# Kernel tuning notes

Measured on AMD Instinct MI355X. Metric: run time of the kernel, lower is better.

## Reference

```python
import jax, jax.numpy as jnp
import numpy as np

N = 131072   # query points
K = 32       # top-k gaussians per point
G = 100000   # num_gaussians
DELTA = 0.05
EPS = 1e-8


def setup_inputs() -> dict:
    key = jax.random.key(0)
    ks = jax.random.split(key, 7)
    coords = jax.random.normal(ks[0], (N, 3), jnp.float32) * 2.0
    # PSF covariance: symmetric PSD per point (A A^T + 0.1 I)
    A = jax.random.normal(ks[1], (N, 3, 3), jnp.float32) * 0.3
    Sigma_psf = jnp.einsum('nij,nkj->nik', A, A) + 0.1 * jnp.eye(3, dtype=jnp.float32)
    mu = jax.random.normal(ks[2], (G, 3), jnp.float32) * 2.0
    scaling = jax.random.uniform(ks[3], (G, 3), jnp.float32, minval=0.5, maxval=1.5)
    rotation_g = jax.random.normal(ks[4], (G, 4), jnp.float32)
    color = jax.random.uniform(ks[5], (G,), jnp.float32)
    top_k_idcs = jax.random.randint(ks[6], (N, K), 0, G)
    return {"coords": coords, "Sigma_psf": Sigma_psf, "mu": mu, "scaling": scaling,
            "rotation_g": rotation_g, "color": color, "top_k_idcs": top_k_idcs}


def _quat_to_rot(q):
    # q: (G,4) wxyz -> R: (G,3,3), matches fused kernel math (rsqrt normalize)
    inv_norm = jax.lax.rsqrt(jnp.sum(q * q, axis=-1, keepdims=True) + EPS)
    qn = q * inv_norm
    w, x, y, z = qn[..., 0], qn[..., 1], qn[..., 2], qn[..., 3]
    x2, y2, z2 = x * x, y * y, z * z
    xy, xz, yz = x * y, x * z, y * z
    wx, wy, wz = w * x, w * y, w * z
    r0 = jnp.stack([1.0 - 2.0 * (y2 + z2), 2.0 * (xy - wz), 2.0 * (xz + wy)], axis=-1)
    r1 = jnp.stack([2.0 * (xy + wz), 1.0 - 2.0 * (x2 + z2), 2.0 * (yz - wx)], axis=-1)
    r2 = jnp.stack([2.0 * (xz - wy), 2.0 * (yz + wx), 1.0 - 2.0 * (x2 + y2)], axis=-1)
    return jnp.stack([r0, r1, r2], axis=-2)


def _compute_sigma(scaling, rotation_g, scale_scale):
    # Sigma = R diag(s^2) R^T, s = scaling * scale_scale
    R = _quat_to_rot(rotation_g)            # (G,3,3)
    M = R * (scaling * scale_scale)[:, None, :]  # scale columns
    return jnp.einsum('gik,gjk->gij', M, M)      # (G,3,3)


def _mahalanobis(sig, v):
    # sig: (N,K,3,3) symmetric; v: (N,K,3). Explicit 3x3 inverse, same as torch kernel.
    a = sig[..., 0, 0]; b = sig[..., 0, 1]; c = sig[..., 0, 2]
    e = sig[..., 1, 1]; f = sig[..., 1, 2]
    h = sig[..., 2, 1]; i = sig[..., 2, 2]
    det = a * (e * i - f * h) - b * (b * i - f * c) + c * (b * h - e * c)
    inv_det = 1.0 / (det + EPS)
    inv00 = (e * i - f * h) * inv_det
    inv01 = (c * h - b * i) * inv_det
    inv02 = (b * f - c * e) * inv_det
    inv11 = (a * i - c * c) * inv_det
    inv12 = (c * b - a * f) * inv_det
    inv22 = (a * e - b * b) * inv_det
    vx, vy, vz = v[..., 0], v[..., 1], v[..., 2]
    t0 = inv00 * vx + inv01 * vy + inv02 * vz
    t1 = inv01 * vx + inv11 * vy + inv12 * vz
    t2 = inv02 * vx + inv12 * vy + inv22 * vz
    return vx * t0 + vy * t1 + vz * t2


def reference(coords, Sigma_psf, mu, scaling, rotation_g, color, top_k_idcs):
    scale_scale = 1.0  # default; thresholding branch inactive
    mus = mu[top_k_idcs]                         # (N,K,3)
    x_minus_mu = coords[:, None, :] - mus        # (N,K,3)
    sigmas = _compute_sigma(scaling, rotation_g, scale_scale)[top_k_idcs]  # (N,K,3,3)
    sigmas = (sigmas + Sigma_psf[:, None, :, :]).astype(jnp.float32)
    inner = _mahalanobis(sigmas, x_minus_mu)     # (N,K)
    w = jnp.exp(-0.5 * inner)
    sum_w = jnp.sum(w, axis=1, keepdims=True)
    w_nrmd = w / (sum_w + DELTA)
    intensity = jnp.sum(w_nrmd * color[top_k_idcs], axis=1)  # (N,)
    return intensity
```

## Files before the change

### kernel.cpp

```cpp
#include <hip/hip_runtime.h>
#include <hip/hip_fp16.h>

#define DELTA 0.05f
#define EPS 1e-8f

union H2F { __half2 h; float f; };

__global__ __launch_bounds__(256) void precompute_gauss(
    const float* __restrict__ mu,
    const float* __restrict__ scaling,
    const float* __restrict__ rot,
    const float* __restrict__ color,
    float4* __restrict__ table, int G)
{
    int g = blockIdx.x * blockDim.x + threadIdx.x;
    if (g >= G) return;
    float qw = rot[g*4+0], qx = rot[g*4+1], qy = rot[g*4+2], qz = rot[g*4+3];
    float inv_norm = rsqrtf(qw*qw + qx*qx + qy*qy + qz*qz + EPS);
    qw *= inv_norm; qx *= inv_norm; qy *= inv_norm; qz *= inv_norm;
    float x2 = qx*qx, y2 = qy*qy, z2 = qz*qz;
    float xy = qx*qy, xz = qx*qz, yz = qy*qz;
    float wx = qw*qx, wy = qw*qy, wz = qw*qz;
    float R00 = 1.f - 2.f*(y2 + z2), R01 = 2.f*(xy - wz),       R02 = 2.f*(xz + wy);
    float R10 = 2.f*(xy + wz),       R11 = 1.f - 2.f*(x2 + z2), R12 = 2.f*(yz - wx);
    float R20 = 2.f*(xz - wy),       R21 = 2.f*(yz + wx),       R22 = 1.f - 2.f*(x2 + y2);
    float s0 = scaling[g*3+0], s1 = scaling[g*3+1], s2 = scaling[g*3+2];
    float d0 = s0*s0, d1 = s1*s1, d2 = s2*s2;
    float S00 = R00*R00*d0 + R01*R01*d1 + R02*R02*d2;
    float S01 = R00*R10*d0 + R01*R11*d1 + R02*R12*d2;
    float S02 = R00*R20*d0 + R01*R21*d1 + R02*R22*d2;
    float S11 = R10*R10*d0 + R11*R11*d1 + R12*R12*d2;
    float S12 = R10*R20*d0 + R11*R21*d1 + R12*R22*d2;
    float S22 = R20*R20*d0 + R21*R21*d1 + R22*R22*d2;

    H2F u01, u21, u22, uc;
    u01.h = __floats2half2_rn(S00, S01);
    u21.h = __floats2half2_rn(S02, S11);
    u22.h = __floats2half2_rn(S12, S22);
    uc.h  = __floats2half2_rn(color[g], 0.f);

    float mx = mu[g*3+0], my = mu[g*3+1], mz = mu[g*3+2];
    table[(size_t)g*2+0] = make_float4(mx, my, mz, u01.f);
    table[(size_t)g*2+1] = make_float4(u21.f, u22.f, uc.f, 0.f);
}

__global__ __launch_bounds__(256) void gsvr_main(
    const float* __restrict__ coords,
    const float* __restrict__ psf,
    const int*   __restrict__ idcs,
    const float4* __restrict__ table,
    float* __restrict__ out, int n_pts)
{
    int tid = blockIdx.x * blockDim.x + threadIdx.x;
    int p  = tid >> 5;
    int kk = tid & 31;
    if (p >= n_pts) return;

    int g = __builtin_nontemporal_load(idcs + (size_t)p*32 + kk);

    float4 r0 = table[(size_t)g*2+0];
    float4 r1 = table[(size_t)g*2+1];

    float cx = __builtin_nontemporal_load(coords + (size_t)p*3+0);
    float cy = __builtin_nontemporal_load(coords + (size_t)p*3+1);
    float cz = __builtin_nontemporal_load(coords + (size_t)p*3+2);
    const float* sp = psf + (size_t)p*9;
    float pa = __builtin_nontemporal_load(sp+0);
    float pb = __builtin_nontemporal_load(sp+1);
    float pc = __builtin_nontemporal_load(sp+2);
    float pe = __builtin_nontemporal_load(sp+4);
    float pf = __builtin_nontemporal_load(sp+5);
    float pi = __builtin_nontemporal_load(sp+8);

    H2F u01, u21, u22, uc;
    u01.f = r0.w; u21.f = r1.x; u22.f = r1.y; uc.f = r1.z;
    float2 s01 = __half22float2(u01.h);
    float2 s21 = __half22float2(u21.h);
    float2 s22 = __half22float2(u22.h);
    float  col = __half22float2(uc.h).x;

    float a = s01.x + pa, b = s01.y + pb, c = s21.x + pc;
    float e = s21.y + pe, f = s22.x + pf, i = s22.y + pi;
    float vx = cx - r0.x, vy = cy - r0.y, vz = cz - r0.z;

    float ei_fh = e*i - f*f;
    float det = a*ei_fh - b*(b*i - f*c) + c*(b*f - e*c);
    float inv_det = 1.0f / (det + EPS);
    float i00 = ei_fh * inv_det;
    float i01 = (c*f - b*i) * inv_det;
    float i02 = (b*f - c*e) * inv_det;
    float i11 = (a*i - c*c) * inv_det;
    float i12 = (c*b - a*f) * inv_det;
    float i22 = (a*e - b*b) * inv_det;

    float q0 = i00*vx + i01*vy + i02*vz;
    float q1 = i01*vx + i11*vy + i12*vz;
    float q2 = i02*vx + i12*vy + i22*vz;
    float inner = vx*q0 + vy*q1 + vz*q2;

    float w  = __expf(-0.5f * inner);
    float wc = w * col;

    #pragma unroll
    for (int m = 16; m >= 1; m >>= 1) {
        w  += __shfl_xor(w,  m);
        wc += __shfl_xor(wc, m);
    }
    if (kk == 0) __builtin_nontemporal_store(wc / (w + DELTA), out + p);
}

__global__ __launch_bounds__(256) void gsvr_fallback(
    const float* __restrict__ coords,
    const float* __restrict__ psf,
    const int*   __restrict__ idcs,
    const float* __restrict__ mu,
    const float* __restrict__ scaling,
    const float* __restrict__ rot,
    const float* __restrict__ color,
    float* __restrict__ out, int n_pts)
{
    int tid = blockIdx.x * blockDim.x + threadIdx.x;
    int p  = tid >> 5;
    int kk = tid & 31;
    if (p >= n_pts) return;

    float cx = coords[p*3+0], cy = coords[p*3+1], cz = coords[p*3+2];
    const float* sp = psf + (size_t)p*9;
    float pa = sp[0], pb = sp[1], pc = sp[2], pe = sp[4], pf = sp[5], pi = sp[8];

    int g = idcs[p*32 + kk];
    float qw = rot[g*4+0], qx = rot[g*4+1], qy = rot[g*4+2], qz = rot[g*4+3];
    float inv_norm = rsqrtf(qw*qw + qx*qx + qy*qy + qz*qz + EPS);
    qw *= inv_norm; qx *= inv_norm; qy *= inv_norm; qz *= inv_norm;
    float x2 = qx*qx, y2 = qy*qy, z2 = qz*qz;
    float xy = qx*qy, xz = qx*qz, yz = qy*qz;
    float wx = qw*qx, wy = qw*qy, wz = qw*qz;
    float R00 = 1.f - 2.f*(y2 + z2), R01 = 2.f*(xy - wz),       R02 = 2.f*(xz + wy);
    float R10 = 2.f*(xy + wz),       R11 = 1.f - 2.f*(x2 + z2), R12 = 2.f*(yz - wx);
    float R20 = 2.f*(xz - wy),       R21 = 2.f*(yz + wx),       R22 = 1.f - 2.f*(x2 + y2);
    float s0 = scaling[g*3+0], s1 = scaling[g*3+1], s2 = scaling[g*3+2];
    float dd0 = s0*s0, dd1 = s1*s1, dd2 = s2*s2;
    float S00 = R00*R00*dd0 + R01*R01*dd1 + R02*R02*dd2;
    float S01 = R00*R10*dd0 + R01*R11*dd1 + R02*R12*dd2;
    float S02 = R00*R20*dd0 + R01*R21*dd1 + R02*R22*dd2;
    float S11 = R10*R10*dd0 + R11*R11*dd1 + R12*R12*dd2;
    float S12 = R10*R20*dd0 + R11*R21*dd1 + R12*R22*dd2;
    float S22 = R20*R20*dd0 + R21*R21*dd1 + R22*R22*dd2;

    float a = S00 + pa, b = S01 + pb, c = S02 + pc;
    float e = S11 + pe, f = S12 + pf, i = S22 + pi;
    float vx = cx - mu[g*3+0], vy = cy - mu[g*3+1], vz = cz - mu[g*3+2];

    float ei_fh = e*i - f*f;
    float det = a*ei_fh - b*(b*i - f*c) + c*(b*f - e*c);
    float inv_det = 1.0f / (det + EPS);
    float i00 = ei_fh * inv_det;
    float i01 = (c*f - b*i) * inv_det;
    float i02 = (b*f - c*e) * inv_det;
    float i11 = (a*i - c*c) * inv_det;
    float i12 = (c*b - a*f) * inv_det;
    float i22 = (a*e - b*b) * inv_det;

    float q0 = i00*vx + i01*vy + i02*vz;
    float q1 = i01*vx + i11*vy + i12*vz;
    float q2 = i02*vx + i12*vy + i22*vz;
    float inner = vx*q0 + vy*q1 + vz*q2;

    float w  = __expf(-0.5f * inner);
    float wc = w * color[g];

    #pragma unroll
    for (int m = 16; m >= 1; m >>= 1) {
        w  += __shfl_xor(w,  m);
        wc += __shfl_xor(wc, m);
    }
    if (kk == 0) out[p] = wc / (w + DELTA);
}

extern "C" void kernel_launch(void* const* d_in, const int* in_sizes, int n_in,
                              void* d_out, int out_size, void* d_ws, size_t ws_size,
                              hipStream_t stream)
{
    const float* coords  = (const float*)d_in[0];
    const float* psf     = (const float*)d_in[1];
    const float* mu      = (const float*)d_in[2];
    const float* scaling = (const float*)d_in[3];
    const float* rot     = (const float*)d_in[4];
    const float* color   = (const float*)d_in[5];
    const int*   idcs    = (const int*)d_in[6];
    float* out = (float*)d_out;

    int n_pts = in_sizes[0] / 3;
    int G     = in_sizes[5];

    size_t need = (size_t)G * 8 * sizeof(float);

    if (ws_size >= need) {
        float4* table = (float4*)d_ws;
        precompute_gauss<<<(G + 255) / 256, 256, 0, stream>>>(mu, scaling, rot, color, table, G);
        int threads = n_pts * 32;
        gsvr_main<<<(threads + 255) / 256, 256, 0, stream>>>(
            coords, psf, idcs, table, out, n_pts);
    } else {
        int threads = n_pts * 32;
        gsvr_fallback<<<(threads + 255) / 256, 256, 0, stream>>>(
            coords, psf, idcs, mu, scaling, rot, color, out, n_pts);
    }
}
```

Before: 45.84 us.

## Split gaussian table row loads across lane pairs and exchange via shuffles

```diff
diff --git a/kernel.cpp b/kernel.cpp
--- a/kernel.cpp
+++ b/kernel.cpp
@@ -44,33 +44,47 @@
     table[(size_t)g*2+1] = make_float4(u21.f, u22.f, uc.f, 0.f);
 }
 
-__global__ __launch_bounds__(256) void gsvr_main(
+__global__ __launch_bounds__(256) void gsvr_dual(
     const float* __restrict__ coords,
     const float* __restrict__ psf,
     const int*   __restrict__ idcs,
     const float4* __restrict__ table,
     float* __restrict__ out, int n_pts)
 {
-    int tid = blockIdx.x * blockDim.x + threadIdx.x;
-    int p  = tid >> 5;
-    int kk = tid & 31;
-    if (p >= n_pts) return;
-
-    int g = __builtin_nontemporal_load(idcs + (size_t)p*32 + kk);
-
-    float4 r0 = table[(size_t)g*2+0];
-    float4 r1 = table[(size_t)g*2+1];
-
-    float cx = __builtin_nontemporal_load(coords + (size_t)p*3+0);
-    float cy = __builtin_nontemporal_load(coords + (size_t)p*3+1);
-    float cz = __builtin_nontemporal_load(coords + (size_t)p*3+2);
-    const float* sp = psf + (size_t)p*9;
+    int tid    = blockIdx.x * blockDim.x + threadIdx.x;
+    int waveId = tid >> 6;
+    int lane   = tid & 63;
+    int pA     = waveId * 2;
+    if (pA >= n_pts) return;
+    int pB     = min(pA + 1, n_pts - 1);
+    int parity = lane & 1;
+    int t      = lane >> 1;
+
+    int gA = __builtin_nontemporal_load(idcs + (size_t)pA*32 + t);
+    int gB = __builtin_nontemporal_load(idcs + (size_t)pB*32 + t);
+
+    float4 vA = table[(size_t)gA*2 + parity];
+    float4 vB = table[(size_t)gB*2 + parity];
+
+    int pm = parity ? pB : pA;
+    float cx = __builtin_nontemporal_load(coords + (size_t)pm*3+0);
+    float cy = __builtin_nontemporal_load(coords + (size_t)pm*3+1);
+    float cz = __builtin_nontemporal_load(coords + (size_t)pm*3+2);
+    const float* sp = psf + (size_t)pm*9;
     float pa = __builtin_nontemporal_load(sp+0);
     float pb = __builtin_nontemporal_load(sp+1);
     float pc = __builtin_nontemporal_load(sp+2);
     float pe = __builtin_nontemporal_load(sp+4);
     float pf = __builtin_nontemporal_load(sp+5);
     float pi = __builtin_nontemporal_load(sp+8);
+
+    float4 oA, oB;
+    oA.x = __shfl_xor(vA.x, 1); oA.y = __shfl_xor(vA.y, 1);
+    oA.z = __shfl_xor(vA.z, 1); oA.w = __shfl_xor(vA.w, 1);
+    oB.x = __shfl_xor(vB.x, 1); oB.y = __shfl_xor(vB.y, 1);
+    oB.z = __shfl_xor(vB.z, 1); oB.w = __shfl_xor(vB.w, 1);
+    float4 r0 = parity ? oB : vA;
+    float4 r1 = parity ? vB : oA;
 
     H2F u01, u21, u22, uc;
     u01.f = r0.w; u21.f = r1.x; u22.f = r1.y; uc.f = r1.z;
@@ -102,11 +116,13 @@
     float wc = w * col;
 
     #pragma unroll
-    for (int m = 16; m >= 1; m >>= 1) {
+    for (int m = 32; m >= 2; m >>= 1) {
         w  += __shfl_xor(w,  m);
         wc += __shfl_xor(wc, m);
     }
-    if (kk == 0) __builtin_nontemporal_store(wc / (w + DELTA), out + p);
+    int po = pA + lane;
+    if (lane < 2 && po < n_pts)
+        __builtin_nontemporal_store(wc / (w + DELTA), out + po);
 }
 
 __global__ __launch_bounds__(256) void gsvr_fallback(
@@ -198,8 +214,9 @@
     if (ws_size >= need) {
         float4* table = (float4*)d_ws;
         precompute_gauss<<<(G + 255) / 256, 256, 0, stream>>>(mu, scaling, rot, color, table, G);
-        int threads = n_pts * 32;
-        gsvr_main<<<(threads + 255) / 256, 256, 0, stream>>>(
+        long long waves   = ((long long)n_pts + 1) / 2;
+        long long threads = waves * 64;
+        gsvr_dual<<<(int)((threads + 255) / 256), 256, 0, stream>>>(
             coords, psf, idcs, table, out, n_pts);
     } else {
         int threads = n_pts * 32;
```

New measurement: 45.33 us. No clear change (-1.1%).
